# Optimization experiments

Hardware: AMD Instinct MI355X
Metric: run time of the kernel (lower is better)

Reference implementation:

```python
import jax, jax.numpy as jnp
import numpy as np
import math

SQRT2 = math.sqrt(2.0)
SQRT_2PI = math.sqrt(2.0 * math.pi)
T = 1.0


def _margin_from_bn(xt_flat):
    # xt_flat: [B, C*L]. torch .std() is unbiased (ddof=1).
    std = jnp.abs(jnp.std(xt_flat, axis=1, ddof=1))  # [B]
    mean = jnp.mean(xt_flat, axis=1)                  # [B]
    z = -mean / std
    cdf = 0.5 * (1.0 + jax.lax.erf(z / SQRT2))        # norm.cdf(-mean/std)
    safe_cdf = jnp.maximum(cdf, 1e-30)                # guard div; branch selected by where
    margin_a = -std * jnp.exp(-(mean / std) ** 2 / 2.0) / SQRT_2PI / safe_cdf + mean
    margin = jnp.where(cdf > 0.001, margin_a, -3.0 * std)
    # original detaches margin (computed on CPU via numpy/scipy)
    return jax.lax.stop_gradient(margin)


def reference(x_s, x_t, x_ts, x_st, i):
    B, C = x_ts.shape[0], x_ts.shape[1]
    xs = x_ts.reshape(B, C, -1)  # source: [B, C, L]
    xt = x_st.reshape(B, C, -1)  # target: [B, C, L]
    margin = _margin_from_bn(xt.reshape(B, -1))  # [B]
    # distillation_loss(source=xs, target=xt, T, dims=1, margin)
    target = jnp.maximum(xt / T, margin[:, None, None])
    entropy = jax.nn.softmax(xs / T, axis=1) * jax.nn.log_softmax(target / T, axis=1)
    channel_entropy = -jnp.sum(entropy, axis=1)          # [B, L]
    batch_mean_entropy = jnp.mean(channel_entropy, axis=1)  # [B]
    loss = jnp.mean(batch_mean_entropy)
    return (loss, entropy)


def setup_inputs() -> dict:
    key = jax.random.key(0)
    k1, k2, k3, k4 = jax.random.split(key, 4)
    return {
        "x_s": jax.random.normal(k1, (1,), dtype=jnp.float32),
        "x_t": jax.random.normal(k2, (1,), dtype=jnp.float32),
        "x_ts": jax.random.normal(k3, (8, 1024, 64, 64), dtype=jnp.float32),
        "x_st": jax.random.normal(k4, (8, 1024, 64, 64), dtype=jnp.float32),
        "i": 0,
    }
```

## Files before the change

kernel.cpp:

```cpp
#include <hip/hip_runtime.h>
#include <math.h>

#define BB 8
#define CC 1024
#define LL 4096
#define NPB (CC*LL)
#define LT 32

typedef float f32x4 __attribute__((ext_vector_type(4)));


__global__ void k_batch_sums(const float* __restrict__ xt, double* __restrict__ sums) {
    int b = blockIdx.y;
    const float4* p = (const float4*)(xt + (size_t)b * NPB);
    int t = blockIdx.x * blockDim.x + threadIdx.x;
    double s1 = 0.0, s2 = 0.0;
    #pragma unroll
    for (int j4 = 0; j4 < 4; ++j4) {
        float4 v[4];
        #pragma unroll
        for (int k = 0; k < 4; ++k) v[k] = p[(size_t)(j4 * 4 + k) * 65536 + t];
        #pragma unroll
        for (int k = 0; k < 4; ++k) {
            float q1 = (v[k].x + v[k].y) + (v[k].z + v[k].w);
            float q2 = (v[k].x * v[k].x + v[k].y * v[k].y)
                     + (v[k].z * v[k].z + v[k].w * v[k].w);
            s1 += (double)q1;
            s2 += (double)q2;
        }
    }
    for (int off = 32; off; off >>= 1) {
        s1 += __shfl_down(s1, off, 64);
        s2 += __shfl_down(s2, off, 64);
    }
    __shared__ double ls1[4], ls2[4];
    int lane = threadIdx.x & 63, w = threadIdx.x >> 6;
    if (lane == 0) { ls1[w] = s1; ls2[w] = s2; }
    __syncthreads();
    if (threadIdx.x == 0) {
        atomicAdd(&sums[2 * b],     ls1[0] + ls1[1] + ls1[2] + ls1[3]);
        atomicAdd(&sums[2 * b + 1], ls2[0] + ls2[1] + ls2[2] + ls2[3]);
    }
}

__global__ __attribute__((amdgpu_flat_work_group_size(1024, 1024), amdgpu_waves_per_eu(4, 4)))
void k_fused(const float* __restrict__ xs, const float* __restrict__ xt,
             const double* __restrict__ sums,
             float* __restrict__ out1, double* __restrict__ lossAcc) {
    int tid = threadIdx.x;
    int b = blockIdx.y;
    int L0 = blockIdx.x * LT;
    int q = tid & 7;
    int g = tid >> 3;
    int lane = tid & 63, w = tid >> 6;

    __shared__ float s_mg;
    __shared__ __align__(16) float s_red[2][16][8][4];
    __shared__ __align__(16) float s_sinv[8][4];
    __shared__ __align__(16) float s_blog[8][4];
    __shared__ float wacc[16];

    if (tid == 0) {
        double n = (double)NPB;
        double s1 = sums[2 * b], s2 = sums[2 * b + 1];
        double mean = s1 / n;
        double var = (s2 - s1 * s1 / n) / (n - 1.0);
        double sd = sqrt(var);
        double z = -mean / sd;
        double cdf = 0.5 * (1.0 + erf(z / 1.4142135623730951));
        double safe = fmax(cdf, 1e-30);
        double r = mean / sd;
        double ma = -sd * exp(-r * r * 0.5) / 2.5066282746310002 / safe + mean;
        s_mg = (float)((cdf > 0.001) ? ma : -3.0 * sd);
    }
    __syncthreads();
    float mg = s_mg;

    const float* ps = xs + (size_t)b * NPB + L0 + q * 4;
    const float* pt = xt + (size_t)b * NPB + L0 + q * 4;

    f32x4 s4[8];
    float4 t4[8];
    #pragma unroll
    for (int i = 0; i < 8; ++i) {
        size_t off = (size_t)(g + 128 * i) * LL;
        s4[i] = __builtin_nontemporal_load((const f32x4*)(ps + off));
        t4[i] = *(const float4*)(pt + off);
    }
    float4 es[8];
    float ss[4] = {0, 0, 0, 0}, sy[4] = {0, 0, 0, 0};
    #pragma unroll
    for (int i = 0; i < 8; ++i) {
        float4 e;
        e.x = __expf(s4[i].x); e.y = __expf(s4[i].y);
        e.z = __expf(s4[i].z); e.w = __expf(s4[i].w);
        es[i] = e;
        ss[0] += e.x; ss[1] += e.y; ss[2] += e.z; ss[3] += e.w;
        sy[0] += __expf(fmaxf(t4[i].x, mg)); sy[1] += __expf(fmaxf(t4[i].y, mg));
        sy[2] += __expf(fmaxf(t4[i].z, mg)); sy[3] += __expf(fmaxf(t4[i].w, mg));
    }
    #pragma unroll
    for (int off = 8; off < 64; off <<= 1) {
        #pragma unroll
        for (int k = 0; k < 4; ++k) {
            ss[k] += __shfl_xor(ss[k], off, 64);
            sy[k] += __shfl_xor(sy[k], off, 64);
        }
    }
    if (lane < 8) {
        #pragma unroll
        for (int k = 0; k < 4; ++k) {
            s_red[0][w][lane][k] = ss[k];
            s_red[1][w][lane][k] = sy[k];
        }
    }
    __syncthreads();
    if (tid < 64) {
        int a  = tid >> 5;
        int qq = (tid >> 2) & 7;
        int k  = tid & 3;
        float t = 0.f;
        #pragma unroll
        for (int ww = 0; ww < 16; ++ww) t += s_red[a][ww][qq][k];
        if (a == 0) s_sinv[qq][k] = 1.0f / t;
        else        s_blog[qq][k] = __logf(t);
    }
    __syncthreads();
    float4 sinv = *(const float4*)&s_sinv[q][0];
    float4 blog = *(const float4*)&s_blog[q][0];

    float* po = out1 + (size_t)b * NPB + L0 + q * 4;
    float4 u4[8];
    #pragma unroll
    for (int i = 0; i < 8; ++i) {
        size_t off = (size_t)(g + 128 * (7 - i)) * LL;
        u4[i] = *(const float4*)(pt + off);
    }
    float acc = 0.f;
    #pragma unroll
    for (int i = 0; i < 8; ++i) {
        int ci = 7 - i;
        size_t off = (size_t)(g + 128 * ci) * LL;
        f32x4 e;
        e.x = es[ci].x * sinv.x * (fmaxf(u4[i].x, mg) - blog.x);
        e.y = es[ci].y * sinv.y * (fmaxf(u4[i].y, mg) - blog.y);
        e.z = es[ci].z * sinv.z * (fmaxf(u4[i].z, mg) - blog.z);
        e.w = es[ci].w * sinv.w * (fmaxf(u4[i].w, mg) - blog.w);
        __builtin_nontemporal_store(e, (f32x4*)(po + off));
        acc += (e.x + e.y) + (e.z + e.w);
    }
    for (int off = 32; off; off >>= 1) acc += __shfl_down(acc, off, 64);
    if (lane == 0) wacc[w] = acc;
    __syncthreads();
    if (tid == 0) {
        double t = 0.0;
        #pragma unroll
        for (int ww = 0; ww < 16; ++ww) t += (double)wacc[ww];
        atomicAdd(lossAcc, t);
    }
}

__global__ void k_finalize(const double* __restrict__ lossAcc, float* __restrict__ out) {
    if (threadIdx.x == 0) out[0] = (float)(-lossAcc[0] / (double)(BB * LL));
}

extern "C" void kernel_launch(void* const* d_in, const int* in_sizes, int n_in,
                              void* d_out, int out_size, void* d_ws, size_t ws_size,
                              hipStream_t stream) {
    const float* x_ts = (const float*)d_in[2];
    const float* x_st = (const float*)d_in[3];
    float* out = (float*)d_out;

    double* sums    = (double*)d_ws;
    double* lossAcc = (double*)((char*)d_ws + 128);

    hipMemsetAsync(d_ws, 0, 256, stream);

    k_batch_sums<<<dim3(256, BB), 256, 0, stream>>>(x_st, sums);
    k_fused<<<dim3(LL / LT, BB), 1024, 0, stream>>>(x_ts, x_st, sums, out + 1, lossAcc);
    k_finalize<<<1, 64, 0, stream>>>(lossAcc, out);
}
```

Baseline: 407.0 us.

## Keep clamped target in fp16 registers instead of reloading xt for output pass

Stores the clamped target values as packed half2 in registers during the first pass, eliminating the second global read of x_st. Also computes the margin per thread after issuing loads and performs the final channel reduction redundantly in every thread to drop a barrier. Saves roughly a third of the fused kernel's memory traffic at the cost of fp16 rounding of targets and extra register pressure and per-thread double math.

```diff
diff --git a/kernel.cpp b/kernel.cpp
--- a/kernel.cpp
+++ b/kernel.cpp
@@ -1,4 +1,5 @@
 #include <hip/hip_runtime.h>
+#include <hip/hip_fp16.h>
 #include <math.h>
 
 #define BB 8
@@ -43,7 +44,7 @@
     }
 }
 
-__global__ __attribute__((amdgpu_flat_work_group_size(1024, 1024), amdgpu_waves_per_eu(4, 4)))
+__global__ __launch_bounds__(1024)
 void k_fused(const float* __restrict__ xs, const float* __restrict__ xt,
              const double* __restrict__ sums,
              float* __restrict__ out1, double* __restrict__ lossAcc) {
@@ -54,27 +55,8 @@
     int g = tid >> 3;
     int lane = tid & 63, w = tid >> 6;
 
-    __shared__ float s_mg;
     __shared__ __align__(16) float s_red[2][16][8][4];
-    __shared__ __align__(16) float s_sinv[8][4];
-    __shared__ __align__(16) float s_blog[8][4];
     __shared__ float wacc[16];
-
-    if (tid == 0) {
-        double n = (double)NPB;
-        double s1 = sums[2 * b], s2 = sums[2 * b + 1];
-        double mean = s1 / n;
-        double var = (s2 - s1 * s1 / n) / (n - 1.0);
-        double sd = sqrt(var);
-        double z = -mean / sd;
-        double cdf = 0.5 * (1.0 + erf(z / 1.4142135623730951));
-        double safe = fmax(cdf, 1e-30);
-        double r = mean / sd;
-        double ma = -sd * exp(-r * r * 0.5) / 2.5066282746310002 / safe + mean;
-        s_mg = (float)((cdf > 0.001) ? ma : -3.0 * sd);
-    }
-    __syncthreads();
-    float mg = s_mg;
 
     const float* ps = xs + (size_t)b * NPB + L0 + q * 4;
     const float* pt = xt + (size_t)b * NPB + L0 + q * 4;
@@ -87,7 +69,24 @@
         s4[i] = __builtin_nontemporal_load((const f32x4*)(ps + off));
         t4[i] = *(const float4*)(pt + off);
     }
+
+    float mg;
+    {
+        double n = (double)NPB;
+        double s1 = sums[2 * b], s2 = sums[2 * b + 1];
+        double mean = s1 / n;
+        double var = (s2 - s1 * s1 / n) / (n - 1.0);
+        double sd = sqrt(var);
+        double z = -mean / sd;
+        double cdf = 0.5 * (1.0 + erf(z / 1.4142135623730951));
+        double safe = fmax(cdf, 1e-30);
+        double r = mean / sd;
+        double ma = -sd * exp(-r * r * 0.5) / 2.5066282746310002 / safe + mean;
+        mg = (float)((cdf > 0.001) ? ma : -3.0 * sd);
+    }
+
     float4 es[8];
+    __half2 yh[16];
     float ss[4] = {0, 0, 0, 0}, sy[4] = {0, 0, 0, 0};
     #pragma unroll
     for (int i = 0; i < 8; ++i) {
@@ -96,8 +95,12 @@
         e.z = __expf(s4[i].z); e.w = __expf(s4[i].w);
         es[i] = e;
         ss[0] += e.x; ss[1] += e.y; ss[2] += e.z; ss[3] += e.w;
-        sy[0] += __expf(fmaxf(t4[i].x, mg)); sy[1] += __expf(fmaxf(t4[i].y, mg));
-        sy[2] += __expf(fmaxf(t4[i].z, mg)); sy[3] += __expf(fmaxf(t4[i].w, mg));
+        float y0 = fmaxf(t4[i].x, mg), y1 = fmaxf(t4[i].y, mg);
+        float y2 = fmaxf(t4[i].z, mg), y3 = fmaxf(t4[i].w, mg);
+        sy[0] += __expf(y0); sy[1] += __expf(y1);
+        sy[2] += __expf(y2); sy[3] += __expf(y3);
+        yh[2 * i]     = __floats2half2_rn(y0, y1);
+        yh[2 * i + 1] = __floats2half2_rn(y2, y3);
     }
     #pragma unroll
     for (int off = 8; off < 64; off <<= 1) {
@@ -115,37 +118,33 @@
         }
     }
     __syncthreads();
-    if (tid < 64) {
-        int a  = tid >> 5;
-        int qq = (tid >> 2) & 7;
-        int k  = tid & 3;
-        float t = 0.f;
-        #pragma unroll
-        for (int ww = 0; ww < 16; ++ww) t += s_red[a][ww][qq][k];
-        if (a == 0) s_sinv[qq][k] = 1.0f / t;
-        else        s_blog[qq][k] = __logf(t);
+
+    float ssT[4] = {0, 0, 0, 0}, syT[4] = {0, 0, 0, 0};
+    #pragma unroll
+    for (int ww = 0; ww < 16; ++ww) {
+        float4 a = *(const float4*)&s_red[0][ww][q][0];
+        float4 c = *(const float4*)&s_red[1][ww][q][0];
+        ssT[0] += a.x; ssT[1] += a.y; ssT[2] += a.z; ssT[3] += a.w;
+        syT[0] += c.x; syT[1] += c.y; syT[2] += c.z; syT[3] += c.w;
     }
-    __syncthreads();
-    float4 sinv = *(const float4*)&s_sinv[q][0];
-    float4 blog = *(const float4*)&s_blog[q][0];
+    float4 sinv, blog;
+    sinv.x = 1.0f / ssT[0]; sinv.y = 1.0f / ssT[1];
+    sinv.z = 1.0f / ssT[2]; sinv.w = 1.0f / ssT[3];
+    blog.x = __logf(syT[0]); blog.y = __logf(syT[1]);
+    blog.z = __logf(syT[2]); blog.w = __logf(syT[3]);
 
     float* po = out1 + (size_t)b * NPB + L0 + q * 4;
-    float4 u4[8];
-    #pragma unroll
-    for (int i = 0; i < 8; ++i) {
-        size_t off = (size_t)(g + 128 * (7 - i)) * LL;
-        u4[i] = *(const float4*)(pt + off);
-    }
     float acc = 0.f;
     #pragma unroll
     for (int i = 0; i < 8; ++i) {
-        int ci = 7 - i;
-        size_t off = (size_t)(g + 128 * ci) * LL;
+        size_t off = (size_t)(g + 128 * i) * LL;
+        float2 ylo = __half22float2(yh[2 * i]);
+        float2 yhi = __half22float2(yh[2 * i + 1]);
         f32x4 e;
-        e.x = es[ci].x * sinv.x * (fmaxf(u4[i].x, mg) - blog.x);
-        e.y = es[ci].y * sinv.y * (fmaxf(u4[i].y, mg) - blog.y);
-        e.z = es[ci].z * sinv.z * (fmaxf(u4[i].z, mg) - blog.z);
-        e.w = es[ci].w * sinv.w * (fmaxf(u4[i].w, mg) - blog.w);
+        e.x = es[i].x * sinv.x * (ylo.x - blog.x);
+        e.y = es[i].y * sinv.y * (ylo.y - blog.y);
+        e.z = es[i].z * sinv.z * (yhi.x - blog.z);
+        e.w = es[i].w * sinv.w * (yhi.y - blog.w);
         __builtin_nontemporal_store(e, (f32x4*)(po + off));
         acc += (e.x + e.y) + (e.z + e.w);
     }
```

Result: no change. 409.6 us (+0.6%).
